# Optimization experiments

Measured on AMD Instinct MI355X. Metric: run time of the kernel, lower is better.

Reference implementation:

```python
import jax, jax.numpy as jnp
import numpy as np

D_MODEL = 1024
H = 16
D_K = D_MODEL // H
D_FF = 4096
EPS = 1e-6
NEG = -1e9


def layernorm(x, alpha, bias):
    # custom LN: unbiased std (ddof=1), scalar alpha/bias, divide by (std+eps)
    mean = jnp.mean(x, axis=-1, keepdims=True)
    n = x.shape[-1]
    var = jnp.sum((x - mean) ** 2, axis=-1, keepdims=True) / (n - 1)
    std = jnp.sqrt(var)
    return alpha * (x - mean) / (std + EPS) + bias


def setup_inputs() -> dict:
    key = jax.random.key(0)
    ks = jax.random.split(key, 16)
    B, S = 2, 2048
    s = 1.0 / np.sqrt(D_MODEL)
    inp = {
        "x": jax.random.normal(ks[0], (B, S, D_MODEL), jnp.float32),
        "src_mask": jnp.ones((B, 1, S), jnp.int32),
        "wq": jax.random.normal(ks[1], (D_MODEL, D_MODEL), jnp.float32) * s,
        "bq": jnp.zeros((D_MODEL,), jnp.float32),
        "wk": jax.random.normal(ks[2], (D_MODEL, D_MODEL), jnp.float32) * s,
        "bk": jnp.zeros((D_MODEL,), jnp.float32),
        "wv": jax.random.normal(ks[3], (D_MODEL, D_MODEL), jnp.float32) * s,
        "bv": jnp.zeros((D_MODEL,), jnp.float32),
        "wo": jax.random.normal(ks[4], (D_MODEL, D_MODEL), jnp.float32) * s,
        "bo": jnp.zeros((D_MODEL,), jnp.float32),
        "w1": jax.random.normal(ks[5], (D_MODEL, D_FF), jnp.float32) * s,
        "b1": jnp.zeros((D_FF,), jnp.float32),
        "w2": jax.random.normal(ks[6], (D_FF, D_MODEL), jnp.float32) * (1.0 / np.sqrt(D_FF)),
        "b2": jnp.zeros((D_MODEL,), jnp.float32),
        "ln1_a": jnp.ones((1,), jnp.float32),
        "ln1_b": jnp.zeros((1,), jnp.float32),
        "ln2_a": jnp.ones((1,), jnp.float32),
        "ln2_b": jnp.zeros((1,), jnp.float32),
    }
    return inp


def reference(x, src_mask, wq, bq, wk, bk, wv, bv, wo, bo,
              w1, b1, w2, b2, ln1_a, ln1_b, ln2_a, ln2_b):
    B, S, _ = x.shape
    # --- residual 1: pre-norm self attention ---
    xn = layernorm(x, ln1_a, ln1_b)
    q = (xn @ wq + bq).reshape(B, S, H, D_K)
    k = (xn @ wk + bk).reshape(B, S, H, D_K)
    v = (xn @ wv + bv).reshape(B, S, H, D_K)
    # scores [B, H, S, S]
    scores = jnp.einsum("bqhd,bkhd->bhqk", q, k) / jnp.sqrt(jnp.float32(D_K))
    m = src_mask[:, None, :, :]  # [B,1,1,S]
    scores = jnp.where(m == 0, NEG, scores)
    attn = jax.nn.softmax(scores, axis=-1)
    ctx = jnp.einsum("bhqk,bkhd->bqhd", attn, v).reshape(B, S, D_MODEL)
    attn_out = ctx @ wo + bo
    x = x + attn_out
    # --- residual 2: pre-norm FFN ---
    xn = layernorm(x, ln2_a, ln2_b)
    ff = jax.nn.relu(xn @ w1 + b1) @ w2 + b2
    return x + ff
```

## Files before the change

kernel.cpp:

```cpp
#include <hip/hip_runtime.h>
#include <hip/hip_bf16.h>

typedef __attribute__((ext_vector_type(8))) short short8;
typedef __attribute__((ext_vector_type(4))) float f32x4;
typedef __attribute__((ext_vector_type(4))) unsigned int u32x4;
using u16 = unsigned short;
typedef unsigned int u32;

__device__ __forceinline__ u16 f2bf(float f) {
    u32 u = __builtin_bit_cast(u32, f);
    u32 r = u + 0x7FFFu + ((u >> 16) & 1u);
    return (u16)(r >> 16);
}

__device__ __forceinline__ float exp2fast(float x) {
    return __builtin_amdgcn_exp2f(x);
}

__device__ __forceinline__ u32 cvtpk(float lo, float hi) {
    u32 r;
    asm("v_cvt_pk_bf16_f32 %0, %1, %2" : "=v"(r) : "v"(lo), "v"(hi));
    return r;
}

__device__ __forceinline__ void async_load16(const void* g, void* l) {
    __builtin_amdgcn_global_load_lds(
        (const __attribute__((address_space(1))) void*)g,
        (__attribute__((address_space(3))) void*)l, 16, 0, 0);
}

__device__ __forceinline__ void wg_barrier() {
    asm volatile("" ::: "memory");
    __builtin_amdgcn_s_barrier();
    asm volatile("" ::: "memory");
}

__global__ __launch_bounds__(256) void convt_kernel(const float* __restrict__ w,
                                                    u16* __restrict__ wt, int K, int N) {
    __shared__ float tile[32][33];
    int bn = blockIdx.x * 32, bk = blockIdx.y * 32;
    int tx = threadIdx.x & 31, ty = threadIdx.x >> 5;
#pragma unroll
    for (int i = 0; i < 4; i++)
        tile[ty + i * 8][tx] = w[(size_t)(bk + ty + i * 8) * N + bn + tx];
    __syncthreads();
#pragma unroll
    for (int i = 0; i < 4; i++)
        wt[(size_t)(bn + ty + i * 8) * K + bk + tx] = f2bf(tile[tx][ty + i * 8]);
}

__global__ __launch_bounds__(256) void convt4_kernel(const float* __restrict__ wa,
                                                     const float* __restrict__ wb,
                                                     const float* __restrict__ wc,
                                                     const float* __restrict__ wd,
                                                     u16* __restrict__ da,
                                                     u16* __restrict__ db,
                                                     u16* __restrict__ dc,
                                                     u16* __restrict__ dd) {
    __shared__ float tile[32][33];
    int z = blockIdx.z;
    const float* w = (z == 0) ? wa : (z == 1) ? wb : (z == 2) ? wc : wd;
    u16* wt = (z == 0) ? da : (z == 1) ? db : (z == 2) ? dc : dd;
    int bn = blockIdx.x * 32, bk = blockIdx.y * 32;
    int tx = threadIdx.x & 31, ty = threadIdx.x >> 5;
#pragma unroll
    for (int i = 0; i < 4; i++)
        tile[ty + i * 8][tx] = w[(size_t)(bk + ty + i * 8) * 1024 + bn + tx];
    __syncthreads();
#pragma unroll
    for (int i = 0; i < 4; i++)
        wt[(size_t)(bn + ty + i * 8) * 1024 + bk + tx] = f2bf(tile[tx][ty + i * 8]);
}

__global__ __launch_bounds__(256) void vtrans_kernel(const u16* __restrict__ qkv,
                                                     u16* __restrict__ vT) {
    __shared__ u16 tile[32][33];
    int bs = blockIdx.x * 32;
    int bc = blockIdx.y * 32;
    int b  = blockIdx.z;
    int tx = threadIdx.x & 31, ty = threadIdx.x >> 5;
#pragma unroll
    for (int i = 0; i < 4; i++)
        tile[ty + i * 8][tx] = qkv[(size_t)(b * 2048 + bs + ty + i * 8) * 3072 + 2048 + bc + tx];
    __syncthreads();
#pragma unroll
    for (int i = 0; i < 4; i++)
        vT[(size_t)(b * 1024 + bc + ty + i * 8) * 2048 + bs + tx] = tile[tx][ty + i * 8];
}

__global__ __launch_bounds__(256) void ln_kernel(const float* __restrict__ x,
                                                 const float* __restrict__ ga,
                                                 const float* __restrict__ gb,
                                                 u16* __restrict__ out) {
    int row = blockIdx.x;
    const float4* xr = (const float4*)(x + (size_t)row * 1024);
    float4 v = xr[threadIdx.x];
    float s  = v.x + v.y + v.z + v.w;
    float s2 = v.x * v.x + v.y * v.y + v.z * v.z + v.w * v.w;
#pragma unroll
    for (int off = 32; off; off >>= 1) {
        s  += __shfl_down(s, off);
        s2 += __shfl_down(s2, off);
    }
    __shared__ float rs[4], rs2[4];
    int wid = threadIdx.x >> 6, lane = threadIdx.x & 63;
    if (lane == 0) { rs[wid] = s; rs2[wid] = s2; }
    __syncthreads();
    float S  = rs[0] + rs[1] + rs[2] + rs[3];
    float S2 = rs2[0] + rs2[1] + rs2[2] + rs2[3];
    float mean = S * (1.0f / 1024.0f);
    float var  = fmaxf((S2 - 1024.0f * mean * mean) * (1.0f / 1023.0f), 0.0f);
    float scale = ga[0] / (sqrtf(var) + 1e-6f);
    float shift = gb[0] - mean * scale;
    u16 h0 = f2bf(v.x * scale + shift);
    u16 h1 = f2bf(v.y * scale + shift);
    u16 h2 = f2bf(v.z * scale + shift);
    u16 h3 = f2bf(v.w * scale + shift);
    uint2 pv;
    pv.x = (u32)h0 | ((u32)h1 << 16);
    pv.y = (u32)h2 | ((u32)h3 << 16);
    *(uint2*)(out + (size_t)row * 1024 + threadIdx.x * 4) = pv;
}

__global__ __launch_bounds__(256) void bias3_kernel(const float* __restrict__ a,
                                                    const float* __restrict__ b,
                                                    const float* __restrict__ c,
                                                    float* __restrict__ d) {
    int i = blockIdx.x * 256 + threadIdx.x;
    float v = (i < 1024) ? a[i] : ((i < 2048) ? b[i - 1024] : c[i - 2048]);
    d[i] = v;
}

__global__ __launch_bounds__(256) void addbias_kernel(float* __restrict__ dst,
                                                      const float* __restrict__ p,
                                                      const float* __restrict__ bias,
                                                      const float* __restrict__ resid) {
    int i4 = blockIdx.x * 256 + threadIdx.x;
    float4 d  = ((const float4*)dst)[i4];
    float4 pp = ((const float4*)p)[i4];
    float4 rr = ((const float4*)resid)[i4];
    float4 bb = *(const float4*)(bias + ((i4 * 4) & 1023));
    d.x += pp.x + bb.x + rr.x;
    d.y += pp.y + bb.y + rr.y;
    d.z += pp.z + bb.z + rr.z;
    d.w += pp.w + bb.w + rr.w;
    ((float4*)dst)[i4] = d;
}

template <int RELU>
__global__ __launch_bounds__(512) void gemm256_bt(const u16* __restrict__ A,
                                                  const u16* __restrict__ Bt,
                                                  const float* __restrict__ bias,
                                                  u16* __restrict__ C,
                                                  int M, int N, int K, int tilesN) {
    __shared__ u16 lds[2][2][16384];
    const int tid = threadIdx.x;
    const int lane = tid & 63, wid = tid >> 6;
    const int l15 = lane & 15, l4 = lane >> 4;
    const int wm = wid >> 2, wn = wid & 3;

    int nwg = gridDim.x;
    int bid = blockIdx.x;
    int swz = (bid & 7) * (nwg >> 3) + (bid >> 3);
    int ty = swz / tilesN, tx = swz % tilesN;

    const u16* Ag = A + (size_t)(ty * 256) * K;
    const u16* Bg = Bt + (size_t)(tx * 256) * K;

    auto stage_half = [&](int slot, int ab, int half, const u16* G, int k0) {
#pragma unroll
        for (int j = 0; j < 2; j++) {
            int off16 = half * 1024 + j * 512 + tid;
            int r = off16 >> 3;
            int gs = (off16 & 7) ^ (r & 7);
            const u16* src = G + (size_t)r * K + k0 + gs * 8;
            u16* dst = &lds[slot][ab][(size_t)(half * 1024 + j * 512 + (wid << 6)) * 8];
            async_load16(src, dst);
        }
    };

    f32x4 acc[8][4] = {};
    const int nT = K >> 6;

    stage_half(0, 0, 0, Ag, 0);
    stage_half(0, 0, 1, Ag, 0);
    stage_half(0, 1, 0, Bg, 0);
    stage_half(0, 1, 1, Bg, 0);
    __builtin_amdgcn_sched_barrier(0);

    for (int t = 0; t < nT; ++t) {
        const int cs = t & 1, ns = cs ^ 1;
        const int k1 = (t + 1) << 6;
        const bool pf = (t + 1 < nT);
#pragma unroll
        for (int ph = 0; ph < 4; ++ph) {
            if (ph == 0 && pf) { stage_half(ns, 0, 0, Ag, k1); stage_half(ns, 0, 1, Ag, k1); }
            if (ph == 1 && pf) { stage_half(ns, 1, 0, Bg, k1); stage_half(ns, 1, 1, Bg, k1); }
            __builtin_amdgcn_sched_barrier(0);
            if (ph == 0) {
                if (pf) asm volatile("s_waitcnt vmcnt(4)" ::: "memory");
                else    asm volatile("s_waitcnt vmcnt(0)" ::: "memory");
            }
            wg_barrier();

            const int rh = ph >> 1, ch = ph & 1;
            const u16* la = &lds[cs][0][0];
            const u16* lb = &lds[cs][1][0];
            short8 af[4][2], bf[2][2];
#pragma unroll
            for (int m2 = 0; m2 < 4; m2++) {
                int ra = wm * 128 + rh * 64 + m2 * 16 + l15;
#pragma unroll
                for (int ks = 0; ks < 2; ks++) {
                    int sl = (l4 + ks * 4) ^ (ra & 7);
                    af[m2][ks] = *(const short8*)&la[ra * 64 + sl * 8];
                }
            }
#pragma unroll
            for (int n2 = 0; n2 < 2; n2++) {
                int rb = wn * 64 + ch * 32 + n2 * 16 + l15;
#pragma unroll
                for (int ks = 0; ks < 2; ks++) {
                    int sl = (l4 + ks * 4) ^ (rb & 7);
                    bf[n2][ks] = *(const short8*)&lb[rb * 64 + sl * 8];
                }
            }
            __builtin_amdgcn_s_setprio(1);
#pragma unroll
            for (int m2 = 0; m2 < 4; m2++)
#pragma unroll
                for (int n2 = 0; n2 < 2; n2++)
#pragma unroll
                    for (int ks = 0; ks < 2; ks++)
                        acc[rh * 4 + m2][ch * 2 + n2] = __builtin_amdgcn_mfma_f32_16x16x32_bf16(
                            af[m2][ks], bf[n2][ks], acc[rh * 4 + m2][ch * 2 + n2], 0, 0, 0);
            __builtin_amdgcn_s_setprio(0);
            wg_barrier();
        }
    }

#pragma unroll
    for (int mi = 0; mi < 8; mi++) {
        int row0 = ty * 256 + wm * 128 + (mi >> 2) * 64 + (mi & 3) * 16 + l4 * 4;
#pragma unroll
        for (int ni = 0; ni < 4; ni++) {
            int col = tx * 256 + wn * 64 + (ni >> 1) * 32 + (ni & 1) * 16 + l15;
            float bc = bias[col];
#pragma unroll
            for (int jj = 0; jj < 4; jj++) {
                float v = acc[mi][ni][jj] + bc;
                if (RELU) v = fmaxf(v, 0.0f);
                C[(size_t)(row0 + jj) * N + col] = f2bf(v);
            }
        }
    }
}

template <int MODE, int RELU, int RESID>
__global__ __launch_bounds__(256) void gemm_bt(const u16* __restrict__ A,
                                               const u16* __restrict__ Bt,
                                               const float* __restrict__ bias,
                                               void* __restrict__ C0,
                                               void* __restrict__ C1,
                                               const float* __restrict__ resid,
                                               int M, int N, int K, int kLen) {
    __shared__ u16 As[8192];
    __shared__ u16 Bs[8192];
    int tid = threadIdx.x, lane = tid & 63, wid = tid >> 6;
    int l15 = lane & 15, l4 = lane >> 4;
    int rowA0 = blockIdx.x * 128;
    int rowB0 = blockIdx.y * 128;
    int kOff = blockIdx.z * kLen;
    void* Cout = blockIdx.z ? C1 : C0;
    int waveM = wid >> 1, waveN = wid & 1;

    int fl = tid * 8;
    int r0 = fl >> 5, c0 = fl & 31;
    const u16* gA0 = A + (size_t)(rowA0 + r0) * K + c0 + kOff;
    const u16* gA1 = A + (size_t)(rowA0 + 64 + r0) * K + c0 + kOff;
    const u16* gB0 = Bt + (size_t)(rowB0 + r0) * K + c0 + kOff;
    const u16* gB1 = Bt + (size_t)(rowB0 + 64 + r0) * K + c0 + kOff;

    f32x4 acc[4][4] = {};
    const int nIter = kLen >> 5;

    async_load16(gA0, As + wid * 512);
    async_load16(gA1, As + 2048 + wid * 512);
    async_load16(gB0, Bs + wid * 512);
    async_load16(gB1, Bs + 2048 + wid * 512);

    int cur = 0, kb = 32;
    for (int it = 0; it < nIter; ++it) {
        asm volatile("s_waitcnt vmcnt(0)" ::: "memory");
        __builtin_amdgcn_s_barrier();
        if (it + 1 < nIter) {
            u16* a = As + (cur ^ 1) * 4096;
            u16* bb = Bs + (cur ^ 1) * 4096;
            async_load16(gA0 + kb, a + wid * 512);
            async_load16(gA1 + kb, a + 2048 + wid * 512);
            async_load16(gB0 + kb, bb + wid * 512);
            async_load16(gB1 + kb, bb + 2048 + wid * 512);
        }
        __builtin_amdgcn_sched_barrier(0);

        const u16* a = As + cur * 4096;
        const u16* bb = Bs + cur * 4096;
        short8 af[4], bf[4];
#pragma unroll
        for (int m = 0; m < 4; m++)
            af[m] = *(const short8*)&a[(waveM * 64 + m * 16 + l15) * 32 + l4 * 8];
#pragma unroll
        for (int n = 0; n < 4; n++)
            bf[n] = *(const short8*)&bb[(waveN * 64 + n * 16 + l15) * 32 + l4 * 8];
#pragma unroll
        for (int m = 0; m < 4; m++)
#pragma unroll
            for (int n = 0; n < 4; n++)
                acc[m][n] = __builtin_amdgcn_mfma_f32_16x16x32_bf16(af[m], bf[n], acc[m][n], 0, 0, 0);

        __builtin_amdgcn_s_barrier();
        cur ^= 1;
        kb += 32;
    }

#pragma unroll
    for (int m = 0; m < 4; m++) {
        int row = rowA0 + waveM * 64 + m * 16 + l4 * 4;
#pragma unroll
        for (int n = 0; n < 4; n++) {
            int col = rowB0 + waveN * 64 + n * 16 + l15;
            float bc = (MODE == 2) ? 0.0f : bias[col];
#pragma unroll
            for (int j = 0; j < 4; j++) {
                float v = acc[m][n][j] + bc;
                if (RELU) v = fmaxf(v, 0.0f);
                if (RESID) v += resid[(size_t)(row + j) * N + col];
                if (MODE == 1)
                    ((u16*)Cout)[(size_t)(row + j) * N + col] = f2bf(v);
                else
                    ((float*)Cout)[(size_t)(row + j) * N + col] = v;
            }
        }
    }
}

__global__ __launch_bounds__(512) void attn_kernel(const u16* __restrict__ qkv,
                                                   const u16* __restrict__ vT,
                                                   const int* __restrict__ mask,
                                                   u16* __restrict__ ctx) {
    const int S = 2048;
    const float C = 0.180336880f;
    int qt = blockIdx.x;
    int bh = blockIdx.y;
    int b = bh >> 4, h = bh & 15;
    int tid = threadIdx.x;
    int wid = tid >> 6, lane = tid & 63;
    int l15 = lane & 15, l4 = lane >> 4;
    int g = wid >> 2, qw = wid & 3;

    __shared__ u16 Ks[2][64][72];
    __shared__ u16 Vs[2][64][72];
    __shared__ u32 PT[8][16][38];
    __shared__ float mbuf[2][4][16], lbuf[2][4][16];
    __shared__ int mflag;

    if (tid == 0) mflag = 1;
    __syncthreads();
    {
        const int* mrow = mask + b * S;
        int ok = 1;
#pragma unroll
        for (int i = 0; i < 4; i++) ok &= (mrow[tid * 4 + i] != 0);
        if (!ok) mflag = 0;
    }

    int qrow0 = qt * 64 + qw * 16;
    const u16* qb = qkv + (size_t)(b * S + qrow0) * 3072 + h * 64;
    short8 qf0 = *(const short8*)(qb + (size_t)l15 * 3072 + l4 * 8);
    short8 qf1 = *(const short8*)(qb + (size_t)l15 * 3072 + 32 + l4 * 8);

    f32x4 o[4] = {};
    float m_i = -1e30f, lp = 0.0f;
    __syncthreads();
    const int allones = mflag;
    const int* mrow = mask + b * S;

    int tl = tid & 255;
    int srow = tl >> 3, c8 = (tl & 7) * 8;
    const int kt0 = g * 16;
    short8 kreg[2], vreg[2];
#pragma unroll
    for (int p = 0; p < 2; p++) {
        int r = p * 32 + srow;
        kreg[p] = *(const short8*)(qkv + (size_t)(b * S + kt0 * 64 + r) * 3072 + 1024 + h * 64 + c8);
        vreg[p] = *(const short8*)(vT + (size_t)(bh * 64 + r) * 2048 + kt0 * 64 + c8);
    }

    for (int it = 0; it < 16; ++it) {
        const int kt = kt0 + it;
        wg_barrier();
#pragma unroll
        for (int p = 0; p < 2; p++) {
            int r = p * 32 + srow;
            *(short8*)&Ks[g][r][c8] = kreg[p];
            *(short8*)&Vs[g][r][c8] = vreg[p];
        }
        if (it + 1 < 16) {
#pragma unroll
            for (int p = 0; p < 2; p++) {
                int r = p * 32 + srow;
                kreg[p] = *(const short8*)(qkv + (size_t)(b * S + (kt + 1) * 64 + r) * 3072 + 1024 + h * 64 + c8);
                vreg[p] = *(const short8*)(vT + (size_t)(bh * 64 + r) * 2048 + (kt + 1) * 64 + c8);
            }
        }
        asm volatile("s_waitcnt lgkmcnt(0)" ::: "memory");
        wg_barrier();

        float sc[4][4];
#pragma unroll
        for (int kc = 0; kc < 4; kc++) {
            short8 kf0 = *(const short8*)&Ks[g][kc * 16 + l15][l4 * 8];
            short8 kf1 = *(const short8*)&Ks[g][kc * 16 + l15][32 + l4 * 8];
            f32x4 a = {};
            a = __builtin_amdgcn_mfma_f32_16x16x32_bf16(kf0, qf0, a, 0, 0, 0);
            a = __builtin_amdgcn_mfma_f32_16x16x32_bf16(kf1, qf1, a, 0, 0, 0);
            if (allones) {
#pragma unroll
                for (int j = 0; j < 4; j++) sc[kc][j] = a[j];
            } else {
#pragma unroll
                for (int j = 0; j < 4; j++) {
                    int mk = mrow[kt * 64 + kc * 16 + l4 * 4 + j];
                    sc[kc][j] = mk ? a[j] : -1e9f;
                }
            }
        }

        float lm = sc[0][0];
#pragma unroll
        for (int kc = 0; kc < 4; kc++)
#pragma unroll
            for (int j = 0; j < 4; j++) lm = fmaxf(lm, sc[kc][j]);
        if (!__all(lm <= m_i + 64.0f)) {
            float t = lm;
            t = fmaxf(t, __shfl_xor(t, 16));
            t = fmaxf(t, __shfl_xor(t, 32));
            float newm = fmaxf(m_i, t);
            float r = exp2fast((m_i - newm) * C);
            lp *= r;
            float rr0 = __shfl(r, l4 * 4 + 0);
            float rr1 = __shfl(r, l4 * 4 + 1);
            float rr2 = __shfl(r, l4 * 4 + 2);
            float rr3 = __shfl(r, l4 * 4 + 3);
#pragma unroll
            for (int dc = 0; dc < 4; dc++) {
                o[dc][0] *= rr0; o[dc][1] *= rr1; o[dc][2] *= rr2; o[dc][3] *= rr3;
            }
            m_i = newm;
        }

        float nb = -m_i * C;
#pragma unroll
        for (int kc = 0; kc < 4; kc++) {
            float p0 = exp2fast(fmaf(sc[kc][0], C, nb));
            float p1 = exp2fast(fmaf(sc[kc][1], C, nb));
            float p2 = exp2fast(fmaf(sc[kc][2], C, nb));
            float p3 = exp2fast(fmaf(sc[kc][3], C, nb));
            lp += (p0 + p1) + (p2 + p3);
            uint2 w;
            w.x = cvtpk(p0, p1);
            w.y = cvtpk(p2, p3);
            *(uint2*)&PT[wid][l15][kc * 8 + l4 * 2] = w;
        }

        uint2 r01 = *(const uint2*)&PT[wid][l15][l4 * 4];
        uint2 r23 = *(const uint2*)&PT[wid][l15][l4 * 4 + 2];
        uint2 r45 = *(const uint2*)&PT[wid][l15][16 + l4 * 4];
        uint2 r67 = *(const uint2*)&PT[wid][l15][16 + l4 * 4 + 2];
        u32x4 w0 = {r01.x, r01.y, r23.x, r23.y};
        u32x4 w1 = {r45.x, r45.y, r67.x, r67.y};
        short8 pa0 = __builtin_bit_cast(short8, w0);
        short8 pa1 = __builtin_bit_cast(short8, w1);

#pragma unroll
        for (int dc = 0; dc < 4; dc++) {
            short8 vf0 = *(const short8*)&Vs[g][dc * 16 + l15][l4 * 8];
            short8 vf1 = *(const short8*)&Vs[g][dc * 16 + l15][32 + l4 * 8];
            o[dc] = __builtin_amdgcn_mfma_f32_16x16x32_bf16(pa0, vf0, o[dc], 0, 0, 0);
            o[dc] = __builtin_amdgcn_mfma_f32_16x16x32_bf16(pa1, vf1, o[dc], 0, 0, 0);
        }
    }

    float lt = lp;
    lt += __shfl_xor(lt, 16);
    lt += __shfl_xor(lt, 32);
    if (l4 == 0) { mbuf[g][qw][l15] = m_i; lbuf[g][qw][l15] = lt; }
    __syncthreads();
    float mo = mbuf[g ^ 1][qw][l15], lo = lbuf[g ^ 1][qw][l15];
    float M  = fmaxf(m_i, mo);
    float rs = exp2fast((m_i - M) * C);
    float ro = exp2fast((mo - M) * C);
    float inv = 1.0f / (rs * lt + ro * lo);
    float rs_j[4], iv_j[4];
#pragma unroll
    for (int j = 0; j < 4; j++) {
        rs_j[j] = __shfl(rs,  l4 * 4 + j);
        iv_j[j] = __shfl(inv, l4 * 4 + j);
    }

    float* obuf = (float*)&Ks[0][0][0];
#pragma unroll
    for (int c = 0; c < 2; c++) {
        int dce = (g ^ 1) * 2 + c;
#pragma unroll
        for (int j = 0; j < 4; j++)
            obuf[(((g * 4 + qw) * 16) + l4 * 4 + j) * 32 + c * 16 + l15] = o[dce][j] * rs_j[j];
    }
    __syncthreads();
#pragma unroll
    for (int c = 0; c < 2; c++) {
        int dco = g * 2 + c;
#pragma unroll
        for (int j = 0; j < 4; j++) {
            float peer = obuf[((((g ^ 1) * 4 + qw) * 16) + l4 * 4 + j) * 32 + c * 16 + l15];
            float val = (o[dco][j] * rs_j[j] + peer) * iv_j[j];
            int row = qrow0 + l4 * 4 + j;
            ctx[(size_t)(b * S + row) * 1024 + h * 64 + dco * 16 + l15] = f2bf(val);
        }
    }
}

extern "C" void kernel_launch(void* const* d_in, const int* in_sizes, int n_in,
                              void* d_out, int out_size, void* d_ws, size_t ws_size,
                              hipStream_t stream) {
    const float* x    = (const float*)d_in[0];
    const int*   mask = (const int*)d_in[1];
    const float* wq   = (const float*)d_in[2];
    const float* bq   = (const float*)d_in[3];
    const float* wk   = (const float*)d_in[4];
    const float* bk   = (const float*)d_in[5];
    const float* wv   = (const float*)d_in[6];
    const float* bv   = (const float*)d_in[7];
    const float* wo   = (const float*)d_in[8];
    const float* bo   = (const float*)d_in[9];
    const float* w1   = (const float*)d_in[10];
    const float* b1   = (const float*)d_in[11];
    const float* w2   = (const float*)d_in[12];
    const float* b2   = (const float*)d_in[13];
    const float* ln1a = (const float*)d_in[14];
    const float* ln1b = (const float*)d_in[15];
    const float* ln2a = (const float*)d_in[16];
    const float* ln2b = (const float*)d_in[17];
    float* out = (float*)d_out;

    char* ws = (char*)d_ws;
    u16*   wqkvt = (u16*)(ws + 0);
    u16*   wot   = (u16*)(ws + 6291456);
    u16*   w1t   = (u16*)(ws + 8388608);
    u16*   w2t   = (u16*)(ws + 16777216);
    float* bqkv  = (float*)(ws + 25165824);
    char*  regA  = ws + 26214400;
    u16*   xn1   = (u16*)(regA + 0);
    u16*   vT    = (u16*)(regA + 0);
    u16*   qkv   = (u16*)(regA + 8388608);
    u16*   ctx   = (u16*)(regA + 33554432);
    float* p0wo  = (float*)(regA + 0);
    float* x1    = (float*)(ws + 68157440);
    u16*   xn2   = (u16*)(regA + 0);
    u16*   ff1   = (u16*)(regA + 8388608);
    float* p0f2  = (float*)(ws + 0);

    dim3 blk(256);

    convt4_kernel<<<dim3(32, 32, 4), blk, 0, stream>>>(
        wq, wk, wv, wo, wqkvt, wqkvt + 1024 * 1024, wqkvt + 2048 * 1024, wot);
    convt_kernel<<<dim3(128, 32), blk, 0, stream>>>(w1, w1t, 1024, 4096);
    convt_kernel<<<dim3(32, 128), blk, 0, stream>>>(w2, w2t, 4096, 1024);
    bias3_kernel<<<dim3(12), blk, 0, stream>>>(bq, bk, bv, bqkv);

    ln_kernel<<<dim3(4096), blk, 0, stream>>>(x, ln1a, ln1b, xn1);
    gemm256_bt<0><<<dim3(192), dim3(512), 0, stream>>>(xn1, wqkvt, bqkv, qkv, 4096, 3072, 1024, 12);
    vtrans_kernel<<<dim3(64, 32, 2), blk, 0, stream>>>(qkv, vT);
    attn_kernel<<<dim3(32, 32), dim3(512), 0, stream>>>(qkv, vT, mask, ctx);
    gemm_bt<2, 0, 0><<<dim3(32, 8, 2), blk, 0, stream>>>(ctx, wot, nullptr, p0wo, x1, nullptr,
                                                         4096, 1024, 1024, 512);
    addbias_kernel<<<dim3(4096), blk, 0, stream>>>(x1, p0wo, bo, x);

    ln_kernel<<<dim3(4096), blk, 0, stream>>>(x1, ln2a, ln2b, xn2);
    gemm256_bt<1><<<dim3(256), dim3(512), 0, stream>>>(xn2, w1t, b1, ff1, 4096, 4096, 1024, 16);
    gemm_bt<2, 0, 0><<<dim3(32, 8, 2), blk, 0, stream>>>(ff1, w2t, nullptr, p0f2, out, nullptr,
                                                         4096, 1024, 4096, 2048);
    addbias_kernel<<<dim3(4096), blk, 0, stream>>>(out, p0f2, b2, x1);
}
```

Before: 270.5 us.

## Alias attention P staging into K tile LDS and split Wo GEMM three ways

The attention kernel drops its dedicated PT shared buffer. It now stages the bf16 probability tile in the K tile region of its wave group, guarded by a new workgroup barrier. This cuts LDS per block, which may allow more resident blocks, but adds a barrier on every key iteration. Separately, the output projection GEMM uses three K splits instead of two, with uneven chunk lengths, and a new epilogue kernel sums two partial buffers plus bias and residual. That adds blocks for parallelism at the cost of writing and reading one more fp32 partial buffer.

```diff
diff --git a/kernel.cpp b/kernel.cpp
--- a/kernel.cpp
+++ b/kernel.cpp
@@ -147,6 +147,24 @@
     ((float4*)dst)[i4] = d;
 }
 
+__global__ __launch_bounds__(256) void addbias2_kernel(float* __restrict__ dst,
+                                                       const float* __restrict__ p0,
+                                                       const float* __restrict__ p1,
+                                                       const float* __restrict__ bias,
+                                                       const float* __restrict__ resid) {
+    int i4 = blockIdx.x * 256 + threadIdx.x;
+    float4 d  = ((const float4*)dst)[i4];
+    float4 pa = ((const float4*)p0)[i4];
+    float4 pb = ((const float4*)p1)[i4];
+    float4 rr = ((const float4*)resid)[i4];
+    float4 bb = *(const float4*)(bias + ((i4 * 4) & 1023));
+    d.x += pa.x + pb.x + bb.x + rr.x;
+    d.y += pa.y + pb.y + bb.y + rr.y;
+    d.z += pa.z + pb.z + bb.z + rr.z;
+    d.w += pa.w + pb.w + bb.w + rr.w;
+    ((float4*)dst)[i4] = d;
+}
+
 template <int RELU>
 __global__ __launch_bounds__(512) void gemm256_bt(const u16* __restrict__ A,
                                                   const u16* __restrict__ Bt,
@@ -262,6 +280,7 @@
                                                const float* __restrict__ bias,
                                                void* __restrict__ C0,
                                                void* __restrict__ C1,
+                                               void* __restrict__ Cp1,
                                                const float* __restrict__ resid,
                                                int M, int N, int K, int kLen) {
     __shared__ u16 As[8192];
@@ -271,7 +290,8 @@
     int rowA0 = blockIdx.x * 128;
     int rowB0 = blockIdx.y * 128;
     int kOff = blockIdx.z * kLen;
-    void* Cout = blockIdx.z ? C1 : C0;
+    int len = K - kOff; if (len > kLen) len = kLen;
+    void* Cout = (blockIdx.z == gridDim.z - 1) ? C1 : (blockIdx.z == 0 ? C0 : Cp1);
     int waveM = wid >> 1, waveN = wid & 1;
 
     int fl = tid * 8;
@@ -282,7 +302,7 @@
     const u16* gB1 = Bt + (size_t)(rowB0 + 64 + r0) * K + c0 + kOff;
 
     f32x4 acc[4][4] = {};
-    const int nIter = kLen >> 5;
+    const int nIter = len >> 5;
 
     async_load16(gA0, As + wid * 512);
     async_load16(gA1, As + 2048 + wid * 512);
@@ -360,9 +380,10 @@
 
     __shared__ u16 Ks[2][64][72];
     __shared__ u16 Vs[2][64][72];
-    __shared__ u32 PT[8][16][38];
     __shared__ float mbuf[2][4][16], lbuf[2][4][16];
     __shared__ int mflag;
+
+    u32* PTw = (u32*)&Ks[g][0][0] + qw * 576;
 
     if (tid == 0) mflag = 1;
     __syncthreads();
@@ -460,6 +481,7 @@
         }
 
         float nb = -m_i * C;
+        u32 pk[4][2];
 #pragma unroll
         for (int kc = 0; kc < 4; kc++) {
             float p0 = exp2fast(fmaf(sc[kc][0], C, nb));
@@ -467,16 +489,24 @@
             float p2 = exp2fast(fmaf(sc[kc][2], C, nb));
             float p3 = exp2fast(fmaf(sc[kc][3], C, nb));
             lp += (p0 + p1) + (p2 + p3);
+            pk[kc][0] = cvtpk(p0, p1);
+            pk[kc][1] = cvtpk(p2, p3);
+        }
+
+        wg_barrier();
+
+#pragma unroll
+        for (int kc = 0; kc < 4; kc++) {
             uint2 w;
-            w.x = cvtpk(p0, p1);
-            w.y = cvtpk(p2, p3);
-            *(uint2*)&PT[wid][l15][kc * 8 + l4 * 2] = w;
-        }
-
-        uint2 r01 = *(const uint2*)&PT[wid][l15][l4 * 4];
-        uint2 r23 = *(const uint2*)&PT[wid][l15][l4 * 4 + 2];
-        uint2 r45 = *(const uint2*)&PT[wid][l15][16 + l4 * 4];
-        uint2 r67 = *(const uint2*)&PT[wid][l15][16 + l4 * 4 + 2];
+            w.x = pk[kc][0];
+            w.y = pk[kc][1];
+            *(uint2*)&PTw[l15 * 36 + kc * 8 + l4 * 2] = w;
+        }
+
+        uint2 r01 = *(const uint2*)&PTw[l15 * 36 + l4 * 4];
+        uint2 r23 = *(const uint2*)&PTw[l15 * 36 + l4 * 4 + 2];
+        uint2 r45 = *(const uint2*)&PTw[l15 * 36 + 16 + l4 * 4];
+        uint2 r67 = *(const uint2*)&PTw[l15 * 36 + 16 + l4 * 4 + 2];
         u32x4 w0 = {r01.x, r01.y, r23.x, r23.y};
         u32x4 w1 = {r45.x, r45.y, r67.x, r67.y};
         short8 pa0 = __builtin_bit_cast(short8, w0);
@@ -565,6 +595,7 @@
     u16*   qkv   = (u16*)(regA + 8388608);
     u16*   ctx   = (u16*)(regA + 33554432);
     float* p0wo  = (float*)(regA + 0);
+    float* p1wo  = (float*)(regA + 16777216);
     float* x1    = (float*)(ws + 68157440);
     u16*   xn2   = (u16*)(regA + 0);
     u16*   ff1   = (u16*)(regA + 8388608);
@@ -582,13 +613,13 @@
     gemm256_bt<0><<<dim3(192), dim3(512), 0, stream>>>(xn1, wqkvt, bqkv, qkv, 4096, 3072, 1024, 12);
     vtrans_kernel<<<dim3(64, 32, 2), blk, 0, stream>>>(qkv, vT);
     attn_kernel<<<dim3(32, 32), dim3(512), 0, stream>>>(qkv, vT, mask, ctx);
-    gemm_bt<2, 0, 0><<<dim3(32, 8, 2), blk, 0, stream>>>(ctx, wot, nullptr, p0wo, x1, nullptr,
-                                                         4096, 1024, 1024, 512);
-    addbias_kernel<<<dim3(4096), blk, 0, stream>>>(x1, p0wo, bo, x);
+    gemm_bt<2, 0, 0><<<dim3(32, 8, 3), blk, 0, stream>>>(ctx, wot, nullptr, p0wo, x1, p1wo,
+                                                         nullptr, 4096, 1024, 1024, 352);
+    addbias2_kernel<<<dim3(4096), blk, 0, stream>>>(x1, p0wo, p1wo, bo, x);
 
     ln_kernel<<<dim3(4096), blk, 0, stream>>>(x1, ln2a, ln2b, xn2);
     gemm256_bt<1><<<dim3(256), dim3(512), 0, stream>>>(xn2, w1t, b1, ff1, 4096, 4096, 1024, 16);
     gemm_bt<2, 0, 0><<<dim3(32, 8, 2), blk, 0, stream>>>(ff1, w2t, nullptr, p0f2, out, nullptr,
-                                                         4096, 1024, 4096, 2048);
+                                                         nullptr, 4096, 1024, 4096, 2048);
     addbias_kernel<<<dim3(4096), blk, 0, stream>>>(out, p0f2, b2, x1);
 }
```

New measurement: 279.8 us. +3.4%, slower.

## Shrink attention KV tile to 32 keys and generalize split-K GEMM outputs

Applied to the files above, without the earlier changes.

The attention kernel now streams K/V in 32-key tiles over 32 iterations instead of 64-key tiles over 16. Shared memory shrinks and each thread holds fewer prefetch registers, which may help occupancy, but there are twice as many barriers and the softmax/PV step per tile is shorter. The split-K GEMM gains a third output pointer and handles a tail chunk, though launches still use the same two-way split, so that path is unchanged.

```diff
diff --git a/kernel.cpp b/kernel.cpp
--- a/kernel.cpp
+++ b/kernel.cpp
@@ -262,6 +262,7 @@
                                                const float* __restrict__ bias,
                                                void* __restrict__ C0,
                                                void* __restrict__ C1,
+                                               void* __restrict__ Cp1,
                                                const float* __restrict__ resid,
                                                int M, int N, int K, int kLen) {
     __shared__ u16 As[8192];
@@ -271,7 +272,8 @@
     int rowA0 = blockIdx.x * 128;
     int rowB0 = blockIdx.y * 128;
     int kOff = blockIdx.z * kLen;
-    void* Cout = blockIdx.z ? C1 : C0;
+    int len = K - kOff; if (len > kLen) len = kLen;
+    void* Cout = (blockIdx.z == gridDim.z - 1) ? C1 : (blockIdx.z == 0 ? C0 : Cp1);
     int waveM = wid >> 1, waveN = wid & 1;
 
     int fl = tid * 8;
@@ -282,7 +284,7 @@
     const u16* gB1 = Bt + (size_t)(rowB0 + 64 + r0) * K + c0 + kOff;
 
     f32x4 acc[4][4] = {};
-    const int nIter = kLen >> 5;
+    const int nIter = len >> 5;
 
     async_load16(gA0, As + wid * 512);
     async_load16(gA1, As + 2048 + wid * 512);
@@ -358,9 +360,10 @@
     int l15 = lane & 15, l4 = lane >> 4;
     int g = wid >> 2, qw = wid & 3;
 
-    __shared__ u16 Ks[2][64][72];
-    __shared__ u16 Vs[2][64][72];
-    __shared__ u32 PT[8][16][38];
+    __shared__ unsigned char KVraw[2 * 32 * 72 * 2 + 2 * 64 * 40 * 2];
+    u16 (*Kts)[32][72] = (u16(*)[32][72])KVraw;
+    u16 (*Vts)[64][40] = (u16(*)[64][40])(KVraw + 9216);
+    __shared__ u32 PT[8][16][36];
     __shared__ float mbuf[2][4][16], lbuf[2][4][16];
     __shared__ int mflag;
 
@@ -387,40 +390,29 @@
 
     int tl = tid & 255;
     int srow = tl >> 3, c8 = (tl & 7) * 8;
-    const int kt0 = g * 16;
-    short8 kreg[2], vreg[2];
-#pragma unroll
-    for (int p = 0; p < 2; p++) {
-        int r = p * 32 + srow;
-        kreg[p] = *(const short8*)(qkv + (size_t)(b * S + kt0 * 64 + r) * 3072 + 1024 + h * 64 + c8);
-        vreg[p] = *(const short8*)(vT + (size_t)(bh * 64 + r) * 2048 + kt0 * 64 + c8);
-    }
-
-    for (int it = 0; it < 16; ++it) {
+    int vrow = tl >> 2, vc8 = (tl & 3) * 8;
+    const int kt0 = g * 32;
+    short8 kreg, vreg;
+    kreg = *(const short8*)(qkv + (size_t)(b * S + kt0 * 32 + srow) * 3072 + 1024 + h * 64 + c8);
+    vreg = *(const short8*)(vT + (size_t)(bh * 64 + vrow) * 2048 + kt0 * 32 + vc8);
+
+    for (int it = 0; it < 32; ++it) {
         const int kt = kt0 + it;
         wg_barrier();
-#pragma unroll
-        for (int p = 0; p < 2; p++) {
-            int r = p * 32 + srow;
-            *(short8*)&Ks[g][r][c8] = kreg[p];
-            *(short8*)&Vs[g][r][c8] = vreg[p];
-        }
-        if (it + 1 < 16) {
-#pragma unroll
-            for (int p = 0; p < 2; p++) {
-                int r = p * 32 + srow;
-                kreg[p] = *(const short8*)(qkv + (size_t)(b * S + (kt + 1) * 64 + r) * 3072 + 1024 + h * 64 + c8);
-                vreg[p] = *(const short8*)(vT + (size_t)(bh * 64 + r) * 2048 + (kt + 1) * 64 + c8);
-            }
+        *(short8*)&Kts[g][srow][c8] = kreg;
+        *(short8*)&Vts[g][vrow][vc8] = vreg;
+        if (it + 1 < 32) {
+            kreg = *(const short8*)(qkv + (size_t)(b * S + (kt + 1) * 32 + srow) * 3072 + 1024 + h * 64 + c8);
+            vreg = *(const short8*)(vT + (size_t)(bh * 64 + vrow) * 2048 + (kt + 1) * 32 + vc8);
         }
         asm volatile("s_waitcnt lgkmcnt(0)" ::: "memory");
         wg_barrier();
 
-        float sc[4][4];
-#pragma unroll
-        for (int kc = 0; kc < 4; kc++) {
-            short8 kf0 = *(const short8*)&Ks[g][kc * 16 + l15][l4 * 8];
-            short8 kf1 = *(const short8*)&Ks[g][kc * 16 + l15][32 + l4 * 8];
+        float sc[2][4];
+#pragma unroll
+        for (int kc = 0; kc < 2; kc++) {
+            short8 kf0 = *(const short8*)&Kts[g][kc * 16 + l15][l4 * 8];
+            short8 kf1 = *(const short8*)&Kts[g][kc * 16 + l15][32 + l4 * 8];
             f32x4 a = {};
             a = __builtin_amdgcn_mfma_f32_16x16x32_bf16(kf0, qf0, a, 0, 0, 0);
             a = __builtin_amdgcn_mfma_f32_16x16x32_bf16(kf1, qf1, a, 0, 0, 0);
@@ -430,17 +422,14 @@
             } else {
 #pragma unroll
                 for (int j = 0; j < 4; j++) {
-                    int mk = mrow[kt * 64 + kc * 16 + l4 * 4 + j];
+                    int mk = mrow[kt * 32 + kc * 16 + l4 * 4 + j];
                     sc[kc][j] = mk ? a[j] : -1e9f;
                 }
             }
         }
 
-        float lm = sc[0][0];
-#pragma unroll
-        for (int kc = 0; kc < 4; kc++)
-#pragma unroll
-            for (int j = 0; j < 4; j++) lm = fmaxf(lm, sc[kc][j]);
+        float lm = fmaxf(fmaxf(fmaxf(sc[0][0], sc[0][1]), fmaxf(sc[0][2], sc[0][3])),
+                         fmaxf(fmaxf(sc[1][0], sc[1][1]), fmaxf(sc[1][2], sc[1][3])));
         if (!__all(lm <= m_i + 64.0f)) {
             float t = lm;
             t = fmaxf(t, __shfl_xor(t, 16));
@@ -461,7 +450,7 @@
 
         float nb = -m_i * C;
 #pragma unroll
-        for (int kc = 0; kc < 4; kc++) {
+        for (int kc = 0; kc < 2; kc++) {
             float p0 = exp2fast(fmaf(sc[kc][0], C, nb));
             float p1 = exp2fast(fmaf(sc[kc][1], C, nb));
             float p2 = exp2fast(fmaf(sc[kc][2], C, nb));
@@ -475,19 +464,13 @@
 
         uint2 r01 = *(const uint2*)&PT[wid][l15][l4 * 4];
         uint2 r23 = *(const uint2*)&PT[wid][l15][l4 * 4 + 2];
-        uint2 r45 = *(const uint2*)&PT[wid][l15][16 + l4 * 4];
-        uint2 r67 = *(const uint2*)&PT[wid][l15][16 + l4 * 4 + 2];
         u32x4 w0 = {r01.x, r01.y, r23.x, r23.y};
-        u32x4 w1 = {r45.x, r45.y, r67.x, r67.y};
         short8 pa0 = __builtin_bit_cast(short8, w0);
-        short8 pa1 = __builtin_bit_cast(short8, w1);
 
 #pragma unroll
         for (int dc = 0; dc < 4; dc++) {
-            short8 vf0 = *(const short8*)&Vs[g][dc * 16 + l15][l4 * 8];
-            short8 vf1 = *(const short8*)&Vs[g][dc * 16 + l15][32 + l4 * 8];
+            short8 vf0 = *(const short8*)&Vts[g][dc * 16 + l15][l4 * 8];
             o[dc] = __builtin_amdgcn_mfma_f32_16x16x32_bf16(pa0, vf0, o[dc], 0, 0, 0);
-            o[dc] = __builtin_amdgcn_mfma_f32_16x16x32_bf16(pa1, vf1, o[dc], 0, 0, 0);
         }
     }
 
@@ -508,7 +491,7 @@
         iv_j[j] = __shfl(inv, l4 * 4 + j);
     }
 
-    float* obuf = (float*)&Ks[0][0][0];
+    float* obuf = (float*)KVraw;
 #pragma unroll
     for (int c = 0; c < 2; c++) {
         int dce = (g ^ 1) * 2 + c;
@@ -583,12 +566,12 @@
     vtrans_kernel<<<dim3(64, 32, 2), blk, 0, stream>>>(qkv, vT);
     attn_kernel<<<dim3(32, 32), dim3(512), 0, stream>>>(qkv, vT, mask, ctx);
     gemm_bt<2, 0, 0><<<dim3(32, 8, 2), blk, 0, stream>>>(ctx, wot, nullptr, p0wo, x1, nullptr,
-                                                         4096, 1024, 1024, 512);
+                                                         nullptr, 4096, 1024, 1024, 512);
     addbias_kernel<<<dim3(4096), blk, 0, stream>>>(x1, p0wo, bo, x);
 
     ln_kernel<<<dim3(4096), blk, 0, stream>>>(x1, ln2a, ln2b, xn2);
     gemm256_bt<1><<<dim3(256), dim3(512), 0, stream>>>(xn2, w1t, b1, ff1, 4096, 4096, 1024, 16);
     gemm_bt<2, 0, 0><<<dim3(32, 8, 2), blk, 0, stream>>>(ff1, w2t, nullptr, p0f2, out, nullptr,
-                                                         4096, 1024, 4096, 2048);
+                                                         nullptr, 4096, 1024, 4096, 2048);
     addbias_kernel<<<dim3(4096), blk, 0, stream>>>(out, p0f2, b2, x1);
 }
```

After: 274.8 us. About the same (+1.6%).
